# Kernel tuning notes

Hardware: AMD Instinct MI355X
Metric: run time of the kernel (lower is better)

Reference implementation:

```python
import jax, jax.numpy as jnp
import numpy as np

DET_SIZE = 5120
DET_THRESHOLD = 0.5
NMS_THRESHOLD = 0.4
STRIDES = (8, 16, 32)
NUM_ANCHORS = 2
TOP_K = 2048  # fixed pre-NMS candidate count (jit-friendly stand-in for torch.where filtering)


def _anchor_centers(stride):
    n = DET_SIZE // stride
    g = jnp.arange(n, dtype=jnp.float32) * stride
    X, Y = jnp.meshgrid(g, g, indexing='xy')       # matches torch.meshgrid(..., indexing='xy')
    c = jnp.stack([X, Y], axis=-1).reshape(-1, 2)  # (n*n, 2), x fastest
    return jnp.repeat(c, NUM_ANCHORS, axis=0)      # stack([c]*2, dim=1).reshape(-1,2) == interleaved repeat


def _pairwise_iou(b):
    # b: (K,4) xyxy
    area = jnp.clip(b[:, 2] - b[:, 0], 0.0) * jnp.clip(b[:, 3] - b[:, 1], 0.0)
    lt = jnp.maximum(b[:, None, :2], b[None, :, :2])
    rb = jnp.minimum(b[:, None, 2:], b[None, :, 2:])
    wh = jnp.clip(rb - lt, 0.0)
    inter = wh[..., 0] * wh[..., 1]
    return inter / (area[:, None] + area[None, :] - inter + 1e-9)


def _forward(scores8, bbox8, lms8, scores16, bbox16, lms16, scores32, bbox32, lms32, det_scale):
    confs, boxes, lmss = [], [], []
    per_stride = [(scores8, bbox8, lms8), (scores16, bbox16, lms16), (scores32, bbox32, lms32)]
    for (conf, bbox, lms), stride in zip(per_stride, STRIDES):
        c = _anchor_centers(stride)                 # (N,2)
        b = bbox * stride                            # distance-style offsets scaled by stride
        l = lms * stride
        box = jnp.concatenate([c - b[:, :2], c + b[:, 2:4]], axis=-1) / det_scale  # (N,4) xyxy
        pts = (c[:, None, :] + l.reshape(-1, 5, 2)) / det_scale                    # (N,5,2)
        confs.append(conf.reshape(-1)); boxes.append(box); lmss.append(pts)
    conf = jnp.concatenate(confs)
    box = jnp.concatenate(boxes, axis=0)
    pts = jnp.concatenate(lmss, axis=0)
    # score threshold via masking (fixed shapes); below-threshold entries get conf=-1
    conf_m = jnp.where(conf >= DET_THRESHOLD, conf, -1.0)
    top_conf, top_idx = jax.lax.top_k(conf_m, TOP_K)
    top_box = box[top_idx]          # (K,4)
    top_pts = pts[top_idx]          # (K,5,2)
    valid = top_conf >= DET_THRESHOLD
    iou = _pairwise_iou(top_box)    # (K,K)
    later = jnp.arange(TOP_K)
    def body(i, keep):
        supp = (iou[i] > NMS_THRESHOLD) & (later > i) & keep[i] & valid[i]
        return keep & ~supp
    keep = jax.lax.fori_loop(0, TOP_K, body, valid)  # greedy NMS in descending-score order
    m = keep.astype(top_box.dtype)
    # (K, 15) = [conf | bbox(4) | lms(10)], suppressed/invalid rows zeroed
    return jnp.concatenate([(top_conf * m)[:, None], top_box * m[:, None], top_pts.reshape(TOP_K, 10) * m[:, None]], axis=-1)


def setup_inputs() -> dict:
    key = jax.random.key(0)
    ks = jax.random.split(key, 9)
    inp = {}
    for i, s in enumerate(STRIDES):
        n = DET_SIZE // s
        N = n * n * NUM_ANCHORS
        inp[f'scores{s}'] = jax.random.uniform(ks[3 * i], (N,), dtype=jnp.float32)
        inp[f'bbox{s}'] = jax.random.uniform(ks[3 * i + 1], (N, 4), dtype=jnp.float32) * 8.0
        inp[f'lms{s}'] = jax.random.normal(ks[3 * i + 2], (N, 10), dtype=jnp.float32) * 4.0
    inp['det_scale'] = jnp.array(0.5, dtype=jnp.float32)
    return inp


def reference(scores8, bbox8, lms8, scores16, bbox16, lms16, scores32, bbox32, lms32, det_scale):
    return _forward(scores8, bbox8, lms8, scores16, bbox16, lms16, scores32, bbox32, lms32, det_scale)
```

## Files before the change

kernel.cpp:

```cpp
#include <hip/hip_runtime.h>
#include <stdint.h>
#include <stddef.h>

#pragma clang fp contract(off)

#define N8   819200u
#define N16  204800u
#define N32  51200u
#define NTOT 1075200u
#define TOPK 2048
#define CAND_MAX 8192
#define NBIN 8192u
#define BINSHIFT 10
#define NMS_THR 0.4f
#define DET_THR 0.5f

#define OFF_HIST   0u
#define OFF_META   32768u
#define OFF_CAND   32832u
#define OFF_TIDX   98368u
#define OFF_TCONF  106560u
#define OFF_BOX    114752u
#define OFF_DIAGT  147520u
#define OFF_SUPPT  155968u

__device__ __forceinline__ float load_conf(unsigned a, const float* __restrict__ s8,
                                           const float* __restrict__ s16,
                                           const float* __restrict__ s32) {
  if (a < N8) return s8[a];
  if (a < N8 + N16) return s16[a - N8];
  return s32[a - (N8 + N16)];
}

__device__ __forceinline__ void decode(unsigned a,
    const float* __restrict__ b8, const float* __restrict__ l8,
    const float* __restrict__ b16, const float* __restrict__ l16,
    const float* __restrict__ b32, const float* __restrict__ l32,
    float& cx, float& cy, float& s, const float*& bb, const float*& lm) {
  if (a < N8) {
    unsigned cell = a >> 1;
    cx = (float)((cell % 640u) * 8u); cy = (float)((cell / 640u) * 8u);
    s = 8.f; bb = b8 + (size_t)a * 4; lm = l8 + (size_t)a * 10;
  } else if (a < N8 + N16) {
    unsigned loc = a - N8; unsigned cell = loc >> 1;
    cx = (float)((cell % 320u) * 16u); cy = (float)((cell / 320u) * 16u);
    s = 16.f; bb = b16 + (size_t)loc * 4; lm = l16 + (size_t)loc * 10;
  } else {
    unsigned loc = a - (N8 + N16); unsigned cell = loc >> 1;
    cx = (float)((cell % 160u) * 32u); cy = (float)((cell / 160u) * 32u);
    s = 32.f; bb = b32 + (size_t)loc * 4; lm = l32 + (size_t)loc * 10;
  }
}

__global__ void k_hist(const float* __restrict__ s8, const float* __restrict__ s16,
                       const float* __restrict__ s32, unsigned* __restrict__ hist) {
  unsigned i = blockIdx.x * blockDim.x + threadIdx.x;
  unsigned st = gridDim.x * blockDim.x;
  for (unsigned a = i; a < NTOT; a += st) {
    float c = load_conf(a, s8, s16, s32);
    if (c >= DET_THR) {
      unsigned v = (__float_as_uint(c) - 0x3F000000u) >> BINSHIFT;
      if (v > NBIN - 1u) v = NBIN - 1u;
      atomicAdd(&hist[v], 1u);
    }
  }
}

__global__ void __launch_bounds__(1024) k_scan(const unsigned* __restrict__ hist,
                                               unsigned* __restrict__ meta) {
  __shared__ unsigned suf[1024];
  int t = threadIdx.x;
  const unsigned* hp = hist + (size_t)t * 8;
  unsigned s = 0;
  for (int b = 0; b < 8; b++) s += hp[b];
  suf[t] = s;
  __syncthreads();
  for (int d = 1; d < 1024; d <<= 1) {
    unsigned v = (t + d < 1024) ? suf[t + d] : 0u;
    __syncthreads();
    suf[t] += v;
    __syncthreads();
  }
  unsigned total = suf[0];
  unsigned mine = suf[t];
  unsigned nxt = (t < 1023) ? suf[t + 1] : 0u;
  if (total < (unsigned)TOPK) {
    if (t == 0) { meta[0] = 0u; meta[2] = total; }
    return;
  }
  if (mine >= (unsigned)TOPK && nxt < (unsigned)TOPK) {
    unsigned run = nxt, cut = (unsigned)t * 8u;
    for (int b = 7; b >= 0; b--) {
      run += hp[b];
      if (run >= (unsigned)TOPK) { cut = (unsigned)t * 8u + (unsigned)b; break; }
    }
    meta[0] = cut; meta[2] = total;
  }
}

__global__ void k_compact(const float* __restrict__ s8, const float* __restrict__ s16,
                          const float* __restrict__ s32, unsigned* __restrict__ meta,
                          unsigned long long* __restrict__ cand) {
  unsigned cut = meta[0];
  unsigned i = blockIdx.x * blockDim.x + threadIdx.x;
  unsigned st = gridDim.x * blockDim.x;
  for (unsigned a = i; a < NTOT; a += st) {
    float c = load_conf(a, s8, s16, s32);
    if (c >= DET_THR) {
      unsigned b = __float_as_uint(c);
      unsigned v = (b - 0x3F000000u) >> BINSHIFT;
      if (v >= cut) {
        unsigned pos = atomicAdd(&meta[3], 1u);
        if (pos < (unsigned)CAND_MAX)
          cand[pos] = ((unsigned long long)b << 32) |
                      (unsigned long long)(0xFFFFFFFFu - a);
      }
    }
  }
}

__global__ void __launch_bounds__(256) k_rank(
    const unsigned long long* __restrict__ cand, const unsigned* __restrict__ meta,
    const float* __restrict__ b8, const float* __restrict__ l8,
    const float* __restrict__ b16, const float* __restrict__ l16,
    const float* __restrict__ b32, const float* __restrict__ l32,
    const float* __restrict__ dsp,
    unsigned* __restrict__ tidx, float* __restrict__ tconf, float* __restrict__ box) {
  unsigned count = meta[3];
  if (count > (unsigned)CAND_MAX) count = (unsigned)CAND_MAX;
  unsigned wave = blockIdx.x * 4u + (threadIdx.x >> 6);
  unsigned lane = threadIdx.x & 63u;
  if (wave >= count) return;
  unsigned long long my = cand[wave];
  unsigned cnt = 0;
  for (unsigned i = lane; i < count; i += 64u)
    cnt += (cand[i] > my) ? 1u : 0u;
  for (int d = 32; d > 0; d >>= 1) cnt += __shfl_down(cnt, d);
  if (lane == 0 && cnt < (unsigned)TOPK) {
    unsigned r = cnt;
    unsigned a = 0xFFFFFFFFu - (unsigned)(my & 0xFFFFFFFFull);
    float conf = __uint_as_float((unsigned)(my >> 32));
    float cx, cy, s; const float* bb; const float* lm;
    decode(a, b8, l8, b16, l16, b32, l32, cx, cy, s, bb, lm);
    float ds = dsp[0];
    float b0 = bb[0] * s, b1 = bb[1] * s, b2 = bb[2] * s, b3 = bb[3] * s;
    box[r * 4 + 0] = (cx - b0) / ds;
    box[r * 4 + 1] = (cy - b1) / ds;
    box[r * 4 + 2] = (cx + b2) / ds;
    box[r * 4 + 3] = (cy + b3) / ds;
    tidx[r] = a; tconf[r] = conf;
  }
}

__global__ void __launch_bounds__(256) k_supp(const float* __restrict__ box,
                                              unsigned long long* __restrict__ supp64,
                                              unsigned* __restrict__ diagT) {
  int i = blockIdx.x;
  const float4 bi = ((const float4*)box)[i];
  float ai = fmaxf(bi.z - bi.x, 0.f) * fmaxf(bi.w - bi.y, 0.f);
  int tid = threadIdx.x;
  int lane = tid & 63, wv = tid >> 6;
  int c = i >> 5, k = i & 31;
  for (int base = 0; base < TOPK; base += 256) {
    int j = base + tid;
    const float4 bj = ((const float4*)box)[j];
    float aj = fmaxf(bj.z - bj.x, 0.f) * fmaxf(bj.w - bj.y, 0.f);
    float ltx = fmaxf(bi.x, bj.x), lty = fmaxf(bi.y, bj.y);
    float rbx = fminf(bi.z, bj.z), rby = fminf(bi.w, bj.w);
    float w = fmaxf(rbx - ltx, 0.f), h = fmaxf(rby - lty, 0.f);
    float inter = w * h;
    float iou = inter / (ai + aj - inter + 1e-9f);
    bool pred = (iou > NMS_THR) && (j > i);
    unsigned long long word = __ballot(pred);
    int w64 = (base >> 6) + wv;
    if (lane == 0) {
      __builtin_nontemporal_store(word, &supp64[(size_t)c * 1024 + k * 32 + w64]);
      if (w64 == (i >> 6))
        __builtin_nontemporal_store(
            (unsigned)(word >> (((i >> 5) & 1) * 32)), &diagT[k * 64 + c]);
    }
  }
}

__global__ void __launch_bounds__(256, 1) k_nms_out(
    const unsigned* __restrict__ supp_t, const unsigned* __restrict__ diagT,
    const unsigned* __restrict__ meta,
    const unsigned* __restrict__ tidx, const float* __restrict__ tconf,
    const float* __restrict__ b8, const float* __restrict__ l8,
    const float* __restrict__ b16, const float* __restrict__ l16,
    const float* __restrict__ b32, const float* __restrict__ l32,
    const float* __restrict__ dsp, float* __restrict__ out) {
  __shared__ unsigned keepw[64];
  int tid = threadIdx.x;
  if (tid < 64) {
    int l = tid;
    unsigned count = meta[3];
    if (count > (unsigned)TOPK) count = (unsigned)TOPK;
    unsigned lo = (unsigned)l * 32u;
    unsigned kw = (count >= lo + 32u) ? 0xFFFFFFFFu
                : (count <= lo ? 0u : ((1u << (count - lo)) - 1u));
    const unsigned* sp = supp_t + l;
    unsigned dg[32];
#pragma unroll
    for (int k = 0; k < 32; k++) dg[k] = diagT[k * 64 + l];
    unsigned T0[32], T1[32], T2[32], T3[32];

#define LOADT(BUF, CH)                                                        \
  _Pragma("unroll") for (int k = 0; k < 32; k++)                              \
      BUF[k] = sp[(size_t)(unsigned)((CH) * 2048 + k * 64)];

    LOADT(T0, 0) LOADT(T1, 1) LOADT(T2, 2) LOADT(T3, 3)

#define STEP(BUF, CC)                                                         \
  {                                                                           \
    const int ch = (CC);                                                      \
    unsigned w = __builtin_amdgcn_readlane(kw, ch);                           \
    _Pragma("unroll") for (int k = 0; k < 32; k++) {                          \
      unsigned d = __builtin_amdgcn_readlane(dg[k], ch);                      \
      w &= ~(((w >> k) & 1u) ? d : 0u);                                       \
    }                                                                         \
    unsigned acc0 = 0u, acc1 = 0u, acc2 = 0u, acc3 = 0u;                      \
    _Pragma("unroll") for (int q = 0; q < 8; q++) {                           \
      unsigned m0 = (unsigned)((int)(w << (31 - (4 * q + 0))) >> 31);         \
      unsigned m1 = (unsigned)((int)(w << (31 - (4 * q + 1))) >> 31);         \
      unsigned m2 = (unsigned)((int)(w << (31 - (4 * q + 2))) >> 31);         \
      unsigned m3 = (unsigned)((int)(w << (31 - (4 * q + 3))) >> 31);         \
      acc0 |= BUF[4 * q + 0] & m0;                                            \
      acc1 |= BUF[4 * q + 1] & m1;                                            \
      acc2 |= BUF[4 * q + 2] & m2;                                            \
      acc3 |= BUF[4 * q + 3] & m3;                                            \
    }                                                                         \
    kw &= ~((acc0 | acc1) | (acc2 | acc3));                                   \
    if (ch + 4 < 64) { LOADT(BUF, ch + 4) }                                   \
  }

#pragma unroll 1
    for (int c = 0; c < 64; c += 4) {
      STEP(T0, c + 0)
      STEP(T1, c + 1)
      STEP(T2, c + 2)
      STEP(T3, c + 3)
    }
#undef LOADT
#undef STEP
    keepw[l] = kw;
  }
  __syncthreads();
  float ds = dsp[0];
  for (int rr = tid; rr < TOPK; rr += 256) {
    bool kept = (keepw[rr >> 5] >> (rr & 31)) & 1u;
    float o[15];
    if (kept) {
      unsigned a = tidx[rr];
      float cx, cy, s; const float* bb; const float* lm;
      decode(a, b8, l8, b16, l16, b32, l32, cx, cy, s, bb, lm);
      o[0] = tconf[rr];
      float b0 = bb[0] * s, b1 = bb[1] * s, b2 = bb[2] * s, b3 = bb[3] * s;
      o[1] = (cx - b0) / ds;
      o[2] = (cy - b1) / ds;
      o[3] = (cx + b2) / ds;
      o[4] = (cy + b3) / ds;
      for (int p = 0; p < 5; p++) {
        float lx = lm[2 * p] * s, ly = lm[2 * p + 1] * s;
        o[5 + 2 * p] = (cx + lx) / ds;
        o[6 + 2 * p] = (cy + ly) / ds;
      }
    } else {
      for (int cc = 0; cc < 15; cc++) o[cc] = 0.f;
    }
    for (int cc = 0; cc < 15; cc++) out[(size_t)rr * 15 + cc] = o[cc];
  }
}

extern "C" void kernel_launch(void* const* d_in, const int* in_sizes, int n_in,
                              void* d_out, int out_size, void* d_ws, size_t ws_size,
                              hipStream_t stream) {
  const float* s8  = (const float*)d_in[0];
  const float* b8  = (const float*)d_in[1];
  const float* l8  = (const float*)d_in[2];
  const float* s16 = (const float*)d_in[3];
  const float* b16 = (const float*)d_in[4];
  const float* l16 = (const float*)d_in[5];
  const float* s32 = (const float*)d_in[6];
  const float* b32 = (const float*)d_in[7];
  const float* l32 = (const float*)d_in[8];
  const float* dsp = (const float*)d_in[9];
  char* ws = (char*)d_ws;
  unsigned* hist = (unsigned*)(ws + OFF_HIST);
  unsigned* meta = (unsigned*)(ws + OFF_META);
  unsigned long long* cand = (unsigned long long*)(ws + OFF_CAND);
  unsigned* tidx = (unsigned*)(ws + OFF_TIDX);
  float* tconf = (float*)(ws + OFF_TCONF);
  float* box = (float*)(ws + OFF_BOX);
  unsigned* diagT = (unsigned*)(ws + OFF_DIAGT);
  unsigned* supp_t = (unsigned*)(ws + OFF_SUPPT);
  float* out = (float*)d_out;

  hipMemsetAsync(ws, 0, OFF_META + 64, stream);
  k_hist<<<2048, 256, 0, stream>>>(s8, s16, s32, hist);
  k_scan<<<1, 1024, 0, stream>>>(hist, meta);
  k_compact<<<2048, 256, 0, stream>>>(s8, s16, s32, meta, cand);
  k_rank<<<CAND_MAX / 4, 256, 0, stream>>>(cand, meta, b8, l8, b16, l16, b32, l32,
                                           dsp, tidx, tconf, box);
  k_supp<<<TOPK, 256, 0, stream>>>(box, (unsigned long long*)supp_t, diagT);
  k_nms_out<<<1, 256, 0, stream>>>(supp_t, diagT, meta, tidx, tconf,
                                   b8, l8, b16, l16, b32, l32, dsp, out);
}
```

Measured before the change: 130.5 us.

## Replace dense suppression bitmatrix with sparse per-chunk edge lists in NMS

The suppression kernel no longer writes the full dense 2048x2048 bit matrix. For each 32-column chunk it appends only the nonzero off-diagonal 32-bit words to a per-chunk list through atomic counters. The serial NMS kernel walks the chunks in order, resolves each chunk's keep mask from the diagonal block, then scatters suppression bits into later chunks with shared-memory atomicOr, reading only the listed entries. This reduces memory traffic and work in the single-block serial sweep, but adds global atomics in k_supp, per-chunk LDS round-trips, and a variable-length loop. Entries past the 2048-per-chunk cap are silently dropped.

Measured after the change: 132.4 us. Within noise of the previous version (+1.5%).

```diff
diff --git a/kernel.cpp b/kernel.cpp
--- a/kernel.cpp
+++ b/kernel.cpp
@@ -14,15 +14,17 @@
 #define BINSHIFT 10
 #define NMS_THR 0.4f
 #define DET_THR 0.5f
+#define LCAP 2048u
 
 #define OFF_HIST   0u
 #define OFF_META   32768u
-#define OFF_CAND   32832u
-#define OFF_TIDX   98368u
-#define OFF_TCONF  106560u
-#define OFF_BOX    114752u
-#define OFF_DIAGT  147520u
-#define OFF_SUPPT  155968u
+#define OFF_CNT    32832u
+#define OFF_CAND   33088u
+#define OFF_TIDX   98624u
+#define OFF_TCONF  106816u
+#define OFF_BOX    115008u
+#define OFF_DIAGT  147776u
+#define OFF_LIST   155968u
 
 __device__ __forceinline__ float load_conf(unsigned a, const float* __restrict__ s8,
                                            const float* __restrict__ s16,
@@ -153,7 +155,8 @@
 }
 
 __global__ void __launch_bounds__(256) k_supp(const float* __restrict__ box,
-                                              unsigned long long* __restrict__ supp64,
+                                              unsigned long long* __restrict__ listg,
+                                              unsigned* __restrict__ cntg,
                                               unsigned* __restrict__ diagT) {
   int i = blockIdx.x;
   const float4 bi = ((const float4*)box)[i];
@@ -174,76 +177,96 @@
     unsigned long long word = __ballot(pred);
     int w64 = (base >> 6) + wv;
     if (lane == 0) {
-      __builtin_nontemporal_store(word, &supp64[(size_t)c * 1024 + k * 32 + w64]);
       if (w64 == (i >> 6))
         __builtin_nontemporal_store(
             (unsigned)(word >> (((i >> 5) & 1) * 32)), &diagT[k * 64 + c]);
+      unsigned lo32 = (unsigned)word;
+      unsigned hi32 = (unsigned)(word >> 32);
+      int w0 = 2 * w64, w1 = 2 * w64 + 1;
+      if (lo32 != 0u && w0 != c) {
+        unsigned pos = atomicAdd(&cntg[c], 1u);
+        if (pos < LCAP)
+          listg[(size_t)c * LCAP + pos] =
+              ((unsigned long long)lo32 << 32) | (unsigned)((k << 6) | w0);
+      }
+      if (hi32 != 0u && w1 != c) {
+        unsigned pos = atomicAdd(&cntg[c], 1u);
+        if (pos < LCAP)
+          listg[(size_t)c * LCAP + pos] =
+              ((unsigned long long)hi32 << 32) | (unsigned)((k << 6) | w1);
+      }
     }
   }
 }
 
 __global__ void __launch_bounds__(256, 1) k_nms_out(
-    const unsigned* __restrict__ supp_t, const unsigned* __restrict__ diagT,
-    const unsigned* __restrict__ meta,
+    const unsigned long long* __restrict__ listg, const unsigned* __restrict__ cntg,
+    const unsigned* __restrict__ diagT, const unsigned* __restrict__ meta,
     const unsigned* __restrict__ tidx, const float* __restrict__ tconf,
     const float* __restrict__ b8, const float* __restrict__ l8,
     const float* __restrict__ b16, const float* __restrict__ l16,
     const float* __restrict__ b32, const float* __restrict__ l32,
     const float* __restrict__ dsp, float* __restrict__ out) {
   __shared__ unsigned keepw[64];
+  __shared__ unsigned acc[64];
   int tid = threadIdx.x;
   if (tid < 64) {
-    int l = tid;
+    const int l = tid;
     unsigned count = meta[3];
     if (count > (unsigned)TOPK) count = (unsigned)TOPK;
-    unsigned lo = (unsigned)l * 32u;
-    unsigned kw = (count >= lo + 32u) ? 0xFFFFFFFFu
-                : (count <= lo ? 0u : ((1u << (count - lo)) - 1u));
-    const unsigned* sp = supp_t + l;
+    acc[l] = 0u;
     unsigned dg[32];
 #pragma unroll
     for (int k = 0; k < 32; k++) dg[k] = diagT[k * 64 + l];
-    unsigned T0[32], T1[32], T2[32], T3[32];
-
-#define LOADT(BUF, CH)                                                        \
-  _Pragma("unroll") for (int k = 0; k < 32; k++)                              \
-      BUF[k] = sp[(size_t)(unsigned)((CH) * 2048 + k * 64)];
-
-    LOADT(T0, 0) LOADT(T1, 1) LOADT(T2, 2) LOADT(T3, 3)
-
-#define STEP(BUF, CC)                                                         \
+    unsigned cntv = cntg[l];
+    if (cntv > LCAP) cntv = LCAP;
+    unsigned long long p0 = listg[(size_t)0 * LCAP + l];
+    unsigned long long p1 = listg[(size_t)1 * LCAP + l];
+    unsigned long long p2 = listg[(size_t)2 * LCAP + l];
+    unsigned long long p3 = listg[(size_t)3 * LCAP + l];
+
+#define NSTEP(PB, CC)                                                         \
   {                                                                           \
     const int ch = (CC);                                                      \
-    unsigned w = __builtin_amdgcn_readlane(kw, ch);                           \
+    unsigned cnt_c = __builtin_amdgcn_readlane(cntv, ch);                     \
+    unsigned av = acc[ch];                                                    \
+    unsigned a0 = __builtin_amdgcn_readfirstlane(av);                         \
+    unsigned lo_ = (unsigned)ch * 32u;                                        \
+    unsigned init_ = (count >= lo_ + 32u) ? 0xFFFFFFFFu                       \
+                   : (count <= lo_ ? 0u : ((1u << (count - lo_)) - 1u));      \
+    unsigned w_ = init_ & ~a0;                                                \
     _Pragma("unroll") for (int k = 0; k < 32; k++) {                          \
-      unsigned d = __builtin_amdgcn_readlane(dg[k], ch);                      \
-      w &= ~(((w >> k) & 1u) ? d : 0u);                                       \
+      unsigned d_ = __builtin_amdgcn_readlane(dg[k], ch);                     \
+      w_ &= ~(((w_ >> k) & 1u) ? d_ : 0u);                                    \
     }                                                                         \
-    unsigned acc0 = 0u, acc1 = 0u, acc2 = 0u, acc3 = 0u;                      \
-    _Pragma("unroll") for (int q = 0; q < 8; q++) {                           \
-      unsigned m0 = (unsigned)((int)(w << (31 - (4 * q + 0))) >> 31);         \
-      unsigned m1 = (unsigned)((int)(w << (31 - (4 * q + 1))) >> 31);         \
-      unsigned m2 = (unsigned)((int)(w << (31 - (4 * q + 2))) >> 31);         \
-      unsigned m3 = (unsigned)((int)(w << (31 - (4 * q + 3))) >> 31);         \
-      acc0 |= BUF[4 * q + 0] & m0;                                            \
-      acc1 |= BUF[4 * q + 1] & m1;                                            \
-      acc2 |= BUF[4 * q + 2] & m2;                                            \
-      acc3 |= BUF[4 * q + 3] & m3;                                            \
+    if (l == 0) keepw[ch] = w_;                                               \
+    if (cnt_c != 0u) {                                                        \
+      unsigned elo = (unsigned)PB;                                            \
+      unsigned ebits = (unsigned)(PB >> 32);                                  \
+      unsigned we = elo & 63u, ke = (elo >> 6) & 31u;                         \
+      if (((unsigned)l < cnt_c) && ((w_ >> ke) & 1u))                         \
+        atomicOr(&acc[we], ebits);                                            \
+      for (unsigned base = 64u; base < cnt_c; base += 64u) {                  \
+        unsigned idx = base + (unsigned)l;                                    \
+        if (idx < cnt_c) {                                                    \
+          unsigned long long e2 = listg[(size_t)ch * LCAP + idx];             \
+          unsigned lo2 = (unsigned)e2;                                        \
+          if ((w_ >> ((lo2 >> 6) & 31u)) & 1u)                                \
+            atomicOr(&acc[lo2 & 63u], (unsigned)(e2 >> 32));                  \
+        }                                                                     \
+      }                                                                       \
     }                                                                         \
-    kw &= ~((acc0 | acc1) | (acc2 | acc3));                                   \
-    if (ch + 4 < 64) { LOADT(BUF, ch + 4) }                                   \
+    if (ch + 4 < 64) PB = listg[(size_t)(ch + 4) * LCAP + l];                 \
   }
 
 #pragma unroll 1
     for (int c = 0; c < 64; c += 4) {
-      STEP(T0, c + 0)
-      STEP(T1, c + 1)
-      STEP(T2, c + 2)
-      STEP(T3, c + 3)
-    }
-#undef LOADT
-#undef STEP
-    keepw[l] = kw;
+      NSTEP(p0, c + 0)
+      NSTEP(p1, c + 1)
+      NSTEP(p2, c + 2)
+      NSTEP(p3, c + 3)
+    }
+#undef NSTEP
   }
   __syncthreads();
   float ds = dsp[0];
@@ -288,21 +311,22 @@
   char* ws = (char*)d_ws;
   unsigned* hist = (unsigned*)(ws + OFF_HIST);
   unsigned* meta = (unsigned*)(ws + OFF_META);
+  unsigned* cnt = (unsigned*)(ws + OFF_CNT);
   unsigned long long* cand = (unsigned long long*)(ws + OFF_CAND);
   unsigned* tidx = (unsigned*)(ws + OFF_TIDX);
   float* tconf = (float*)(ws + OFF_TCONF);
   float* box = (float*)(ws + OFF_BOX);
   unsigned* diagT = (unsigned*)(ws + OFF_DIAGT);
-  unsigned* supp_t = (unsigned*)(ws + OFF_SUPPT);
+  unsigned long long* listg = (unsigned long long*)(ws + OFF_LIST);
   float* out = (float*)d_out;
 
-  hipMemsetAsync(ws, 0, OFF_META + 64, stream);
+  hipMemsetAsync(ws, 0, OFF_CAND, stream);
   k_hist<<<2048, 256, 0, stream>>>(s8, s16, s32, hist);
   k_scan<<<1, 1024, 0, stream>>>(hist, meta);
   k_compact<<<2048, 256, 0, stream>>>(s8, s16, s32, meta, cand);
   k_rank<<<CAND_MAX / 4, 256, 0, stream>>>(cand, meta, b8, l8, b16, l16, b32, l32,
                                            dsp, tidx, tconf, box);
-  k_supp<<<TOPK, 256, 0, stream>>>(box, (unsigned long long*)supp_t, diagT);
-  k_nms_out<<<1, 256, 0, stream>>>(supp_t, diagT, meta, tidx, tconf,
+  k_supp<<<TOPK, 256, 0, stream>>>(box, listg, cnt, diagT);
+  k_nms_out<<<1, 256, 0, stream>>>(listg, cnt, diagT, meta, tidx, tconf,
                                    b8, l8, b16, l16, b32, l32, dsp, out);
 }
```
